# Kernel tuning notes

Hardware: AMD Instinct MI355X
Metric: run time of the kernel (lower is better)

Reference implementation:

```python
import jax, jax.numpy as jnp
import numpy as np

N_NODES = 50000
N_EDGES = 400000
NFEAT, NHID, NOUT, NCLASS = 512, 256, 256, 8


def _glorot(key, shape):
    lim = float(np.sqrt(6.0 / (shape[0] + shape[1])))
    return jax.random.uniform(key, shape, jnp.float32, -lim, lim)


def setup_inputs() -> dict:
    key = jax.random.key(0)
    ks = jax.random.split(key, 8)
    x = jax.random.normal(ks[0], (N_NODES, NFEAT), jnp.float32)
    edge_index = jax.random.randint(ks[1], (2, N_EDGES), 0, N_NODES, jnp.int32)
    # learnable edge weight logits (init 1 - eps in the module; trained => generic values)
    edge_w_params = jnp.ones((N_EDGES,), jnp.float32) * 0.9999
    W1 = _glorot(ks[2], (NFEAT, NHID)); b1 = jnp.zeros((NHID,), jnp.float32)
    W2 = _glorot(ks[3], (NHID, NHID)); b2 = jnp.zeros((NHID,), jnp.float32)
    W3 = _glorot(ks[4], (NHID, NOUT)); b3 = jnp.zeros((NOUT,), jnp.float32)
    Wlin = _glorot(ks[5], (NHID + NHID + NOUT, NCLASS))
    blin = jnp.zeros((NCLASS,), jnp.float32)
    return {"x": x, "edge_index": edge_index, "edge_w_params": edge_w_params,
            "W1": W1, "b1": b1, "W2": W2, "b2": b2, "W3": W3, "b3": b3,
            "Wlin": Wlin, "blin": blin}


def _gcn_conv(x, W, b, src, dst, ew, n):
    """PyG GCNConv with add_self_loops=True.
    Self-loop weight is 1 (fill_value). norm = d^-1/2[src] * w * d^-1/2[dst].
    Self-loop contribution handled analytically (no edge concat).
    """
    deg = jax.ops.segment_sum(ew, dst, num_segments=n) + 1.0  # +1 self-loop weight
    dinv = jnp.where(deg > 0, jax.lax.rsqrt(deg), 0.0)
    norm = dinv[src] * ew * dinv[dst]                          # [E]
    h = x @ W                                                  # [n, out]
    agg = jax.ops.segment_sum(h[src] * norm[:, None], dst, num_segments=n)
    agg = agg + h * (dinv * dinv)[:, None]                     # self loops
    return agg + b


def reference(x, edge_index, edge_w_params, W1, b1, W2, b2, W3, b3, Wlin, blin):
    n = x.shape[0]
    src, dst = edge_index[0], edge_index[1]
    ew = jax.nn.sigmoid(edge_w_params)
    ones_ew = jnp.ones_like(ew)
    x1 = jax.nn.relu(_gcn_conv(x, W1, b1, src, dst, ew, n))    # dropout: eval mode (identity)
    x2 = jax.nn.relu(_gcn_conv(x1, W2, b2, src, dst, ew, n))
    x3 = _gcn_conv(x2, W3, b3, src, dst, ones_ew, n)           # gc3 called without edge_weight
    logits = jnp.concatenate((x1, x2, x3), axis=1) @ Wlin + blin
    return jax.nn.log_softmax(logits, axis=1)
```

## Files before the change

### kernel.cpp

```cpp
#include <hip/hip_runtime.h>
#include <math.h>

#define N_NODES 50000
#define N_EDGES 400000
#define M_PAD 50048
#define NFEAT 512
#define NHID 256
#define NCLASS 8
#define SCAN_BLOCKS ((N_NODES + 255) / 256)

typedef unsigned short u16;
typedef __attribute__((ext_vector_type(8))) unsigned short u16x8;
typedef __attribute__((ext_vector_type(8))) short s16x8;
typedef __attribute__((ext_vector_type(4))) float f32x4;

__device__ __forceinline__ float bf2f(u16 u) {
    union { unsigned int i; float f; } v; v.i = ((unsigned int)u) << 16; return v.f;
}
__device__ __forceinline__ float bf2f_hi(unsigned int packed) {
    union { unsigned int i; float f; } v; v.i = packed & 0xffff0000u; return v.f;
}
__device__ __forceinline__ float bf2f_lo(unsigned int packed) {
    union { unsigned int i; float f; } v; v.i = packed << 16; return v.f;
}
__device__ __forceinline__ u16 f2bf(float f) {
    union { float f; unsigned int i; } v; v.f = f;
    unsigned int r = v.i + 0x7fffu + ((v.i >> 16) & 1u);
    return (u16)(r >> 16);
}


__global__ void init_k(float* deg, int* cnt, int* cur) {
    int i = blockIdx.x * blockDim.x + threadIdx.x;
    if (i < N_NODES) { deg[i] = 1.0f; cnt[i] = 0; cur[i] = 0; }
}

__global__ void edge_deg_k(const float* __restrict__ p, const int* __restrict__ dst,
                           float* __restrict__ deg, int* __restrict__ cnt,
                           float* __restrict__ ew_out) {
    int e = blockIdx.x * blockDim.x + threadIdx.x;
    if (e >= N_EDGES) return;
    float ew = 1.0f / (1.0f + expf(-p[e]));
    ew_out[e] = ew;
    int d = dst[e];
    atomicAdd(&deg[d], ew);
    atomicAdd(&cnt[d], 1);
}

__global__ void finalize_dinv_k(float* __restrict__ deg, const int* __restrict__ cnt,
                                float* __restrict__ dinv3) {
    int i = blockIdx.x * blockDim.x + threadIdx.x;
    if (i < N_NODES) {
        deg[i]   = 1.0f / sqrtf(deg[i]);
        dinv3[i] = 1.0f / sqrtf(1.0f + (float)cnt[i]);
    }
}

__global__ __launch_bounds__(256) void scan1_k(const int* __restrict__ cnt,
                                               int* __restrict__ row_start,
                                               int* __restrict__ bsum) {
    __shared__ int tmp[256];
    int t = threadIdx.x;
    int g = blockIdx.x * 256 + t;
    int v = (g < N_NODES) ? cnt[g] : 0;
    tmp[t] = v;
    __syncthreads();
    #pragma unroll
    for (int off = 1; off < 256; off <<= 1) {
        int u = (t >= off) ? tmp[t - off] : 0;
        __syncthreads();
        tmp[t] += u;
        __syncthreads();
    }
    if (g < N_NODES) row_start[g] = tmp[t] - v;
    if (t == 255) bsum[blockIdx.x] = tmp[255];
}

__global__ __launch_bounds__(256) void scan2_k(int* __restrict__ bsum) {
    __shared__ int tmp[256];
    int t = threadIdx.x;
    int v = (t < SCAN_BLOCKS) ? bsum[t] : 0;
    tmp[t] = v;
    __syncthreads();
    #pragma unroll
    for (int off = 1; off < 256; off <<= 1) {
        int u = (t >= off) ? tmp[t - off] : 0;
        __syncthreads();
        tmp[t] += u;
        __syncthreads();
    }
    if (t < SCAN_BLOCKS) bsum[t] = tmp[t] - v;
}

__global__ __launch_bounds__(256) void scan3_k(int* __restrict__ row_start,
                                               const int* __restrict__ bsum) {
    int t = threadIdx.x;
    int g = blockIdx.x * 256 + t;
    if (g < N_NODES) row_start[g] += bsum[blockIdx.x];
    if (g == 0) row_start[N_NODES] = N_EDGES;
}

__global__ void fill_k(const int* __restrict__ src, const int* __restrict__ dst,
                       const float* __restrict__ ew, const float* __restrict__ dinv,
                       const float* __restrict__ dinv3,
                       const int* __restrict__ row_start, int* __restrict__ cur,
                       uint2* __restrict__ ep, uint2* __restrict__ ep3) {
    int e = blockIdx.x * blockDim.x + threadIdx.x;
    if (e >= N_EDGES) return;
    int s = src[e], d = dst[e];
    float w  = dinv[s] * ew[e] * dinv[d];
    float w3 = dinv3[s] * dinv3[d];
    int p = atomicAdd(&cur[d], 1);
    int slot = row_start[d] + p;
    ep[slot]  = make_uint2((unsigned int)s, __float_as_uint(w));
    ep3[slot] = make_uint2((unsigned int)s, __float_as_uint(w3));
}


__global__ void wtrans_all_k(const float* __restrict__ W1, const float* __restrict__ W2,
                             const float* __restrict__ W3, u16* __restrict__ wt1,
                             u16* __restrict__ wt2, u16* __restrict__ wt3) {
    int idx = blockIdx.x * 256 + threadIdx.x;
    const float* W; u16* Wt; int K;
    if (idx < 256 * 512)           { W = W1; Wt = wt1; K = 512; }
    else if (idx < 256 * 512 + 256 * 256) { idx -= 256 * 512; W = W2; Wt = wt2; K = 256; }
    else if (idx < 256 * 512 + 2 * 256 * 256) { idx -= 256 * 512 + 256 * 256; W = W3; Wt = wt3; K = 256; }
    else return;
    int n = idx / K, k = idx - n * K;
    Wt[(size_t)n * K + k] = f2bf(W[(size_t)k * 256 + n]);
}

__global__ void zeropad_k(u16* a, u16* b) {
    int i = blockIdx.x * 256 + threadIdx.x;
    if (i < (M_PAD - N_NODES) * 256) {
        a[(size_t)N_NODES * 256 + i] = 0;
        b[(size_t)N_NODES * 256 + i] = 0;
    }
}


__device__ __forceinline__ u16x8 ldcvt_f32(const float* p, bool ok) {
    u16x8 o = {0, 0, 0, 0, 0, 0, 0, 0};
    if (ok) {
        float4 a = *(const float4*)p;
        float4 b = *(const float4*)(p + 4);
        o[0] = f2bf(a.x); o[1] = f2bf(a.y); o[2] = f2bf(a.z); o[3] = f2bf(a.w);
        o[4] = f2bf(b.x); o[5] = f2bf(b.y); o[6] = f2bf(b.z); o[7] = f2bf(b.w);
    }
    return o;
}

template <bool AF32>
__global__ __launch_bounds__(64, 2) void gemm_rr_k(const void* __restrict__ Ap,
                                                   const u16* __restrict__ BT,
                                                   u16* __restrict__ C, int K) {
    int lane = threadIdx.x;
    int row0 = blockIdx.y * 64;
    int col0 = blockIdx.x * 128;
    const u16*   A16 = (const u16*)Ap;
    const float* A32 = (const float*)Ap;

    int fr = lane & 15;
    int kb = (lane >> 4) << 3;

    f32x4 acc[4][8] = {};

    int nt = K >> 5;
    for (int t = 0; t < nt; ++t) {
        int k0 = t * 32 + kb;
        s16x8 af[4];
        #pragma unroll
        for (int m = 0; m < 4; ++m) {
            int gr = row0 + m * 16 + fr;
            if constexpr (AF32) {
                af[m] = (s16x8)ldcvt_f32(A32 + (size_t)gr * K + k0, gr < N_NODES);
            } else {
                af[m] = *(const s16x8*)(A16 + (size_t)gr * K + k0);
            }
        }
        s16x8 bf[8];
        #pragma unroll
        for (int n = 0; n < 8; ++n)
            bf[n] = *(const s16x8*)(BT + (size_t)(col0 + n * 16 + fr) * K + k0);
        #pragma unroll
        for (int m = 0; m < 4; ++m)
            #pragma unroll
            for (int n = 0; n < 8; ++n)
                acc[m][n] = __builtin_amdgcn_mfma_f32_16x16x32_bf16(af[m], bf[n], acc[m][n], 0, 0, 0);
    }

    int crow0 = row0 + ((lane >> 4) << 2);
    int ccol  = col0 + fr;
    #pragma unroll
    for (int m = 0; m < 4; ++m)
        #pragma unroll
        for (int n = 0; n < 8; ++n)
            #pragma unroll
            for (int r = 0; r < 4; ++r)
                C[(size_t)(crow0 + m * 16 + r) * 256 + ccol + n * 16] = f2bf(acc[m][n][r]);
}


template <bool RELU>
__global__ __launch_bounds__(256) void gather_k(const u16* __restrict__ h,
                                                const int* __restrict__ row_start,
                                                const uint2* __restrict__ ep,
                                                const float* __restrict__ dinv,
                                                const float* __restrict__ bias,
                                                u16* __restrict__ outb) {
    int node = blockIdx.x * 4 + (threadIdx.x >> 6);
    if (node >= N_NODES) return;
    int lane = threadIdx.x & 63;

    float di = dinv[node];
    float sw = di * di;
    uint2 hv = *(const uint2*)(h + (size_t)node * 256 + lane * 4);
    float4 acc;
    acc.x = bf2f_lo(hv.x) * sw; acc.y = bf2f_hi(hv.x) * sw;
    acc.z = bf2f_lo(hv.y) * sw; acc.w = bf2f_hi(hv.y) * sw;

    int beg = row_start[node], end = row_start[node + 1];
    int j = beg;
    for (; j + 4 <= end; j += 4) {
        uint2 e0 = ep[j], e1 = ep[j + 1], e2 = ep[j + 2], e3 = ep[j + 3];
        uint2 u0 = *(const uint2*)(h + (size_t)e0.x * 256 + lane * 4);
        uint2 u1 = *(const uint2*)(h + (size_t)e1.x * 256 + lane * 4);
        uint2 u2 = *(const uint2*)(h + (size_t)e2.x * 256 + lane * 4);
        uint2 u3 = *(const uint2*)(h + (size_t)e3.x * 256 + lane * 4);
        float w0 = __uint_as_float(e0.y), w1 = __uint_as_float(e1.y);
        float w2 = __uint_as_float(e2.y), w3 = __uint_as_float(e3.y);
        acc.x += bf2f_lo(u0.x) * w0; acc.y += bf2f_hi(u0.x) * w0;
        acc.z += bf2f_lo(u0.y) * w0; acc.w += bf2f_hi(u0.y) * w0;
        acc.x += bf2f_lo(u1.x) * w1; acc.y += bf2f_hi(u1.x) * w1;
        acc.z += bf2f_lo(u1.y) * w1; acc.w += bf2f_hi(u1.y) * w1;
        acc.x += bf2f_lo(u2.x) * w2; acc.y += bf2f_hi(u2.x) * w2;
        acc.z += bf2f_lo(u2.y) * w2; acc.w += bf2f_hi(u2.y) * w2;
        acc.x += bf2f_lo(u3.x) * w3; acc.y += bf2f_hi(u3.x) * w3;
        acc.z += bf2f_lo(u3.y) * w3; acc.w += bf2f_hi(u3.y) * w3;
    }
    for (; j < end; ++j) {
        uint2 e = ep[j];
        float w = __uint_as_float(e.y);
        uint2 uv = *(const uint2*)(h + (size_t)e.x * 256 + lane * 4);
        acc.x += bf2f_lo(uv.x) * w; acc.y += bf2f_hi(uv.x) * w;
        acc.z += bf2f_lo(uv.y) * w; acc.w += bf2f_hi(uv.y) * w;
    }
    float4 bv = ((const float4*)bias)[lane];
    acc.x += bv.x; acc.y += bv.y; acc.z += bv.z; acc.w += bv.w;
    if (RELU) {
        acc.x = fmaxf(acc.x, 0.f); acc.y = fmaxf(acc.y, 0.f);
        acc.z = fmaxf(acc.z, 0.f); acc.w = fmaxf(acc.w, 0.f);
    }
    uint2 o;
    o.x = (unsigned int)f2bf(acc.x) | ((unsigned int)f2bf(acc.y) << 16);
    o.y = (unsigned int)f2bf(acc.z) | ((unsigned int)f2bf(acc.w) << 16);
    *(uint2*)(outb + (size_t)node * 256 + lane * 4) = o;
}


template <bool FIRST>
__global__ __launch_bounds__(256) void logits_acc_k(const u16* __restrict__ x,
                                                    const float* __restrict__ Wlin,
                                                    const float* __restrict__ blin,
                                                    float* __restrict__ logits, int seg) {
    __shared__ float Ws[256 * 8];
    int tid = threadIdx.x;
    const float* Wseg = Wlin + (size_t)seg * 256 * 8;
    for (int i = tid; i < 2048; i += 256) Ws[i] = Wseg[i];
    __syncthreads();
    int row = blockIdx.x * 32 + (tid >> 3);
    int c = tid & 7;
    if (row >= N_NODES) return;
    const u16* xr = x + (size_t)row * 256;
    float acc = 0.f;
    for (int k8 = 0; k8 < 32; ++k8) {
        u16x8 v = *(const u16x8*)&xr[k8 * 8];
        #pragma unroll
        for (int i = 0; i < 8; ++i) acc += bf2f(v[i]) * Ws[(k8 * 8 + i) * 8 + c];
    }
    float* lp = &logits[(size_t)row * 8 + c];
    if (FIRST) *lp = acc + blin[c];
    else       *lp += acc;
}

__global__ void log_softmax_k(const float* __restrict__ logits, float* __restrict__ out) {
    int row = blockIdx.x * blockDim.x + threadIdx.x;
    if (row >= N_NODES) return;
    float4 a = *(const float4*)&logits[(size_t)row * 8];
    float4 b = *(const float4*)&logits[(size_t)row * 8 + 4];
    float m = fmaxf(fmaxf(fmaxf(a.x, a.y), fmaxf(a.z, a.w)),
                    fmaxf(fmaxf(b.x, b.y), fmaxf(b.z, b.w)));
    float s = expf(a.x - m) + expf(a.y - m) + expf(a.z - m) + expf(a.w - m)
            + expf(b.x - m) + expf(b.y - m) + expf(b.z - m) + expf(b.w - m);
    float ls = logf(s) + m;
    float* o = &out[(size_t)row * 8];
    o[0] = a.x - ls; o[1] = a.y - ls; o[2] = a.z - ls; o[3] = a.w - ls;
    o[4] = b.x - ls; o[5] = b.y - ls; o[6] = b.z - ls; o[7] = b.w - ls;
}


extern "C" void kernel_launch(void* const* d_in, const int* in_sizes, int n_in,
                              void* d_out, int out_size, void* d_ws, size_t ws_size,
                              hipStream_t stream) {
    const float* x    = (const float*)d_in[0];
    const int*   ei   = (const int*)d_in[1];
    const float* ewp  = (const float*)d_in[2];
    const float* W1   = (const float*)d_in[3];
    const float* b1   = (const float*)d_in[4];
    const float* W2   = (const float*)d_in[5];
    const float* b2   = (const float*)d_in[6];
    const float* W3   = (const float*)d_in[7];
    const float* b3   = (const float*)d_in[8];
    const float* Wlin = (const float*)d_in[9];
    const float* blin = (const float*)d_in[10];
    float* out = (float*)d_out;

    const int* src = ei;
    const int* dst = ei + N_EDGES;

    float* ws = (float*)d_ws;
    float* ew     = ws;
    float* dinv   = ew + N_EDGES;
    float* dinv3  = dinv + N_NODES;
    float* logits = dinv3 + N_NODES;
    int* cnt       = (int*)(logits + (size_t)N_NODES * 8);
    int* cur       = cnt + N_NODES;
    int* row_start = cur + N_NODES;
    int* bsum      = row_start + N_NODES + 1;
    uint2* ep  = (uint2*)(((uintptr_t)(bsum + SCAN_BLOCKS) + 127) & ~(uintptr_t)127);
    uint2* ep3 = ep + N_EDGES;
    u16* hb  = (u16*)(ep3 + N_EDGES);
    u16* x1b = hb  + (size_t)M_PAD * 256;
    u16* x2b = x1b + (size_t)M_PAD * 256;
    u16* x3b = x2b + (size_t)M_PAD * 256;
    u16* wt1 = x3b + (size_t)M_PAD * 256;
    u16* wt2 = wt1 + 256 * 512;
    u16* wt3 = wt2 + 256 * 256;

    dim3 blk(256);
    dim3 blk64(64);
    int nodeBlocks  = (N_NODES + 255) / 256;
    int edgeBlocks  = (N_EDGES + 255) / 256;
    int gathBlocks  = (N_NODES + 3) / 4;
    int rowBlocks32 = (N_NODES + 31) / 32;
    dim3 gemmGrid(2, M_PAD / 64);

    init_k<<<nodeBlocks, blk, 0, stream>>>(dinv, cnt, cur);
    edge_deg_k<<<edgeBlocks, blk, 0, stream>>>(ewp, dst, dinv, cnt, ew);
    finalize_dinv_k<<<nodeBlocks, blk, 0, stream>>>(dinv, cnt, dinv3);
    scan1_k<<<SCAN_BLOCKS, blk, 0, stream>>>(cnt, row_start, bsum);
    scan2_k<<<1, blk, 0, stream>>>(bsum);
    scan3_k<<<SCAN_BLOCKS, blk, 0, stream>>>(row_start, bsum);
    fill_k<<<edgeBlocks, blk, 0, stream>>>(src, dst, ew, dinv, dinv3, row_start, cur, ep, ep3);

    wtrans_all_k<<<(256 * 512 + 2 * 256 * 256 + 255) / 256, blk, 0, stream>>>(
        W1, W2, W3, wt1, wt2, wt3);
    zeropad_k<<<48, blk, 0, stream>>>(x1b, x2b);

    gemm_rr_k<true><<<gemmGrid, blk64, 0, stream>>>(x, wt1, hb, NFEAT);
    gather_k<true><<<gathBlocks, blk, 0, stream>>>(hb, row_start, ep, dinv, b1, x1b);
    logits_acc_k<true><<<rowBlocks32, blk, 0, stream>>>(x1b, Wlin, blin, logits, 0);

    gemm_rr_k<false><<<gemmGrid, blk64, 0, stream>>>(x1b, wt2, hb, NHID);
    gather_k<true><<<gathBlocks, blk, 0, stream>>>(hb, row_start, ep, dinv, b2, x2b);
    logits_acc_k<false><<<rowBlocks32, blk, 0, stream>>>(x2b, Wlin, blin, logits, 1);

    gemm_rr_k<false><<<gemmGrid, blk64, 0, stream>>>(x2b, wt3, hb, NHID);
    gather_k<false><<<gathBlocks, blk, 0, stream>>>(hb, row_start, ep3, dinv3, b3, x3b);
    logits_acc_k<false><<<rowBlocks32, blk, 0, stream>>>(x3b, Wlin, blin, logits, 2);

    log_softmax_k<<<nodeBlocks, blk, 0, stream>>>(logits, out);
}
```

Baseline: 343.8 us.

## Shrink GEMM tiles to 32x64 and double-buffer register loads across K

```diff
diff --git a/kernel.cpp b/kernel.cpp
--- a/kernel.cpp
+++ b/kernel.cpp
@@ -150,51 +150,71 @@
     return o;
 }
 
-template <bool AF32>
-__global__ __launch_bounds__(64, 2) void gemm_rr_k(const void* __restrict__ Ap,
-                                                   const u16* __restrict__ BT,
-                                                   u16* __restrict__ C, int K) {
+#define LOADF(AV, BV, T)                                                        \
+    do {                                                                        \
+        _Pragma("unroll")                                                       \
+        for (int m = 0; m < 2; ++m) {                                           \
+            if constexpr (AF32) AV[m] = (s16x8)ldcvt_f32(ap32[m] + (T) * 32, ok[m]); \
+            else                AV[m] = *(const s16x8*)(ap16[m] + (T) * 32);    \
+        }                                                                       \
+        _Pragma("unroll")                                                       \
+        for (int n = 0; n < 4; ++n)                                             \
+            BV[n] = *(const s16x8*)(bp[n] + (T) * 32);                          \
+    } while (0)
+
+#define MFMAF(AV, BV)                                                           \
+    do {                                                                        \
+        _Pragma("unroll")                                                       \
+        for (int m = 0; m < 2; ++m)                                             \
+            _Pragma("unroll")                                                   \
+            for (int n = 0; n < 4; ++n)                                         \
+                acc[m][n] = __builtin_amdgcn_mfma_f32_16x16x32_bf16(AV[m], BV[n], acc[m][n], 0, 0, 0); \
+    } while (0)
+
+template <bool AF32, int MINW>
+__global__ __launch_bounds__(64, MINW) void gemm_rr_k(const void* __restrict__ Ap,
+                                                      const u16* __restrict__ BT,
+                                                      u16* __restrict__ C, int K) {
     int lane = threadIdx.x;
-    int row0 = blockIdx.y * 64;
-    int col0 = blockIdx.x * 128;
+    int row0 = blockIdx.y * 32;
+    int col0 = blockIdx.x * 64;
     const u16*   A16 = (const u16*)Ap;
     const float* A32 = (const float*)Ap;
 
     int fr = lane & 15;
     int kb = (lane >> 4) << 3;
 
-    f32x4 acc[4][8] = {};
+    const u16* ap16[2]; const float* ap32[2]; bool ok[2];
+    #pragma unroll
+    for (int m = 0; m < 2; ++m) {
+        int gr = row0 + m * 16 + fr;
+        ok[m]   = gr < N_NODES;
+        ap16[m] = A16 + (size_t)gr * K + kb;
+        ap32[m] = A32 + (size_t)gr * K + kb;
+    }
+    const u16* bp[4];
+    #pragma unroll
+    for (int n = 0; n < 4; ++n)
+        bp[n] = BT + (size_t)(col0 + n * 16 + fr) * K + kb;
+
+    f32x4 acc[2][4] = {};
+    s16x8 a0[2], b0[4], a1[2], b1[4];
 
     int nt = K >> 5;
-    for (int t = 0; t < nt; ++t) {
-        int k0 = t * 32 + kb;
-        s16x8 af[4];
-        #pragma unroll
-        for (int m = 0; m < 4; ++m) {
-            int gr = row0 + m * 16 + fr;
-            if constexpr (AF32) {
-                af[m] = (s16x8)ldcvt_f32(A32 + (size_t)gr * K + k0, gr < N_NODES);
-            } else {
-                af[m] = *(const s16x8*)(A16 + (size_t)gr * K + k0);
-            }
-        }
-        s16x8 bf[8];
-        #pragma unroll
-        for (int n = 0; n < 8; ++n)
-            bf[n] = *(const s16x8*)(BT + (size_t)(col0 + n * 16 + fr) * K + k0);
-        #pragma unroll
-        for (int m = 0; m < 4; ++m)
-            #pragma unroll
-            for (int n = 0; n < 8; ++n)
-                acc[m][n] = __builtin_amdgcn_mfma_f32_16x16x32_bf16(af[m], bf[n], acc[m][n], 0, 0, 0);
+    LOADF(a0, b0, 0);
+    for (int t = 0; t < nt; t += 2) {
+        LOADF(a1, b1, t + 1);
+        MFMAF(a0, b0);
+        if (t + 2 < nt) LOADF(a0, b0, t + 2);
+        MFMAF(a1, b1);
     }
 
     int crow0 = row0 + ((lane >> 4) << 2);
     int ccol  = col0 + fr;
     #pragma unroll
-    for (int m = 0; m < 4; ++m)
+    for (int m = 0; m < 2; ++m)
         #pragma unroll
-        for (int n = 0; n < 8; ++n)
+        for (int n = 0; n < 4; ++n)
             #pragma unroll
             for (int r = 0; r < 4; ++r)
                 C[(size_t)(crow0 + m * 16 + r) * 256 + ccol + n * 16] = f2bf(acc[m][n][r]);
@@ -343,7 +363,7 @@
     int edgeBlocks  = (N_EDGES + 255) / 256;
     int gathBlocks  = (N_NODES + 3) / 4;
     int rowBlocks32 = (N_NODES + 31) / 32;
-    dim3 gemmGrid(2, M_PAD / 64);
+    dim3 gemmGrid(4, M_PAD / 32);
 
     init_k<<<nodeBlocks, blk, 0, stream>>>(dinv, cnt, cur);
     edge_deg_k<<<edgeBlocks, blk, 0, stream>>>(ewp, dst, dinv, cnt, ew);
@@ -357,15 +377,15 @@
         W1, W2, W3, wt1, wt2, wt3);
     zeropad_k<<<48, blk, 0, stream>>>(x1b, x2b);
 
-    gemm_rr_k<true><<<gemmGrid, blk64, 0, stream>>>(x, wt1, hb, NFEAT);
+    gemm_rr_k<true, 3><<<gemmGrid, blk64, 0, stream>>>(x, wt1, hb, NFEAT);
     gather_k<true><<<gathBlocks, blk, 0, stream>>>(hb, row_start, ep, dinv, b1, x1b);
     logits_acc_k<true><<<rowBlocks32, blk, 0, stream>>>(x1b, Wlin, blin, logits, 0);
 
-    gemm_rr_k<false><<<gemmGrid, blk64, 0, stream>>>(x1b, wt2, hb, NHID);
+    gemm_rr_k<false, 4><<<gemmGrid, blk64, 0, stream>>>(x1b, wt2, hb, NHID);
     gather_k<true><<<gathBlocks, blk, 0, stream>>>(hb, row_start, ep, dinv, b2, x2b);
     logits_acc_k<false><<<rowBlocks32, blk, 0, stream>>>(x2b, Wlin, blin, logits, 1);
 
-    gemm_rr_k<false><<<gemmGrid, blk64, 0, stream>>>(x2b, wt3, hb, NHID);
+    gemm_rr_k<false, 4><<<gemmGrid, blk64, 0, stream>>>(x2b, wt3, hb, NHID);
     gather_k<false><<<gathBlocks, blk, 0, stream>>>(hb, row_start, ep3, dinv3, b3, x3b);
     logits_acc_k<false><<<rowBlocks32, blk, 0, stream>>>(x3b, Wlin, blin, logits, 2);
 
```

After: 409.7 us. 1.19x slower.
